# Kernel optimization log

Hardware: AMD Instinct MI355X
Metric: run time of the kernel (lower is better)

The kernel has to match this reference:

```python
import jax, jax.numpy as jnp
import numpy as np

DIM = 768
HEADS = 12
B, N = 1, 4096


def setup_inputs() -> dict:
    key = jax.random.key(0)
    k1, k2, k3 = jax.random.split(key, 3)
    x = jax.random.normal(k1, (B, N, DIM), dtype=jnp.float32)
    W_qkv = jax.random.normal(k2, (DIM, 3 * DIM), dtype=jnp.float32) * (DIM ** -0.5)
    W_out = jax.random.normal(k3, (DIM, DIM), dtype=jnp.float32) * (DIM ** -0.5)
    b_out = jnp.zeros((DIM,), dtype=jnp.float32)
    return {"x": x, "W_qkv": W_qkv, "W_out": W_out, "b_out": b_out}


def reference(x, W_qkv, W_out, b_out):
    b, n, dim = x.shape
    h = HEADS
    d = dim // h
    qkv = x @ W_qkv  # [b, n, 3*dim]
    q, k, v = jnp.split(qkv, 3, axis=-1)
    # 'b n (h d) -> b h n d'
    def to_heads(a):
        return a.reshape(b, n, h, d).transpose(0, 2, 1, 3)
    q, k, v = to_heads(q), to_heads(k), to_heads(v)
    # NOTE: original module computes self.scale but never applies it -> unscaled dots
    dots = jnp.einsum('bhid,bhjd->bhij', q, k)
    attn = jax.nn.softmax(dots, axis=-1)
    out = jnp.einsum('bhij,bhjd->bhid', attn, v)
    out = out.transpose(0, 2, 1, 3).reshape(b, n, dim)  # 'b h n d -> b n (h d)'
    return out @ W_out + b_out
```

## Files before the change

kernel.cpp:

```cpp
#include <hip/hip_runtime.h>

typedef unsigned short ushort_t;
typedef unsigned int uint_t;
typedef __bf16 bf16x8 __attribute__((ext_vector_type(8)));
typedef __bf16 bf16x4 __attribute__((ext_vector_type(4)));
typedef float f32x4 __attribute__((ext_vector_type(4)));
typedef ushort_t u16x4 __attribute__((ext_vector_type(4)));

#define NSEQ 4096
#define DIMM 768
#define NQKV 2304
#define HEADS 12
#define LOG2E 1.4426950408889634f

#if __has_builtin(__builtin_amdgcn_exp2f)
#define EXP2(x) __builtin_amdgcn_exp2f(x)
#else
#define EXP2(x) exp2f(x)
#endif


__device__ __forceinline__ ushort_t f2bf(float f) {
    uint_t u = __float_as_uint(f);
    u = u + 0x7fffu + ((u >> 16) & 1u);
    return (ushort_t)(u >> 16);
}
__device__ __forceinline__ f32x4 zero4() {
    f32x4 v = {0.f, 0.f, 0.f, 0.f};
    return v;
}

__device__ __forceinline__ void gload_lds16(const ushort_t* g, ushort_t* l) {
    __builtin_amdgcn_global_load_lds(
        (const __attribute__((address_space(1))) void*)g,
        (__attribute__((address_space(3))) void*)l, 16, 0, 0);
}

__device__ __forceinline__ void pack_w_tile(const float* __restrict__ src,
                                            ushort_t* __restrict__ dst,
                                            int K, int N, int bk, int bn, int t,
                                            ushort_t* Ls) {
    const int tr = t >> 4, tc = t & 15;
#pragma unroll
    for (int i = 0; i < 4; ++i) {
        int r = tr + 16 * i;
        float4 v = *(const float4*)(&src[(size_t)(bk + r) * N + bn + tc * 4]);
        const float* vv = (const float*)&v;
#pragma unroll
        for (int j = 0; j < 4; ++j) Ls[(tc * 4 + j) * 72 + r] = f2bf(vv[j]);
    }
    __syncthreads();
    const int KB = K >> 3;
    const int n = t >> 2;
    const int ks = t & 3;
    const int gn = bn + n;
    size_t base = ((size_t)(gn >> 4) * KB + ((bk + ks * 16) >> 3)) * 128 + (gn & 15) * 8;
    *(uint4*)(&dst[base])       = *(const uint4*)(&Ls[n * 72 + ks * 16]);
    *(uint4*)(&dst[base + 128]) = *(const uint4*)(&Ls[n * 72 + ks * 16 + 8]);
}

#define CVT_BLOCKS   3072
#define PW1_BLOCKS   (12 * 36)
#define PW2_BLOCKS   (12 * 12)

__global__ __launch_bounds__(256) void prep_kernel(
    const float* __restrict__ X, const float* __restrict__ Wqkv, const float* __restrict__ Wout,
    ushort_t* __restrict__ Ap, ushort_t* __restrict__ Wqp, ushort_t* __restrict__ Wop)
{
    __shared__ ushort_t Ls[64 * 72];
    const int b = blockIdx.x;
    const int t = threadIdx.x;
    if (b < CVT_BLOCKS) {
        int i = b * 256 + t;
        int row = i / (DIMM / 4);
        int k0 = (i - row * (DIMM / 4)) * 4;
        float4 v = *(const float4*)(&X[(size_t)row * DIMM + k0]);
        u16x4 p = { f2bf(v.x), f2bf(v.y), f2bf(v.z), f2bf(v.w) };
        size_t idx = ((size_t)(row >> 4) * (DIMM / 8) + (k0 >> 3)) * 128 + (row & 15) * 8 + (k0 & 7);
        *(u16x4*)(&Ap[idx]) = p;
    } else if (b < CVT_BLOCKS + PW1_BLOCKS) {
        int j = b - CVT_BLOCKS;
        pack_w_tile(Wqkv, Wqp, DIMM, NQKV, (j % 12) * 64, (j / 12) * 64, t, Ls);
    } else {
        int j = b - CVT_BLOCKS - PW1_BLOCKS;
        pack_w_tile(Wout, Wop, DIMM, DIMM, (j % 12) * 64, (j / 12) * 64, t, Ls);
    }
}

#define QKV_STAGE(buf, kt) do {                                          \
    gload_lds16(asrc0 + (kt) * 512, &As[buf][(w * 2)     * 512]);        \
    gload_lds16(asrc1 + (kt) * 512, &As[buf][(w * 2 + 1) * 512]);        \
    gload_lds16(bsrc0 + (kt) * 512, &Bs[buf][(w * 2)     * 512]);        \
    gload_lds16(bsrc1 + (kt) * 512, &Bs[buf][(w * 2 + 1) * 512]);        \
} while (0)

#define QKV_FRAGS(cur) \
    bf16x8 af[4], bfv[4];                                                \
    _Pragma("unroll")                                                    \
    for (int mi = 0; mi < 4; ++mi)                                       \
        af[mi] = *(const bf16x8*)(&As[cur][aoff + mi * 512 + lfr]);      \
    _Pragma("unroll")                                                    \
    for (int nj = 0; nj < 4; ++nj)                                       \
        bfv[nj] = *(const bf16x8*)(&Bs[cur][boff + nj * 512 + lfr]);

__global__ __launch_bounds__(256) void qkv_gemm_kernel(
    const ushort_t* __restrict__ Ap, const ushort_t* __restrict__ Bp,
    ushort_t* __restrict__ Qp, ushort_t* __restrict__ Kp, ushort_t* __restrict__ Vp)
{
    __shared__ ushort_t As[2][4096], Bs[2][4096];
    const int t = threadIdx.x;
    const int lane = t & 63;
    const int w = t >> 6;
    const int m16 = lane & 15;
    const int g = lane >> 4;
    const int wrow = (w >> 1) * 64;
    const int wcol = (w & 1) * 64;
    const int bm = blockIdx.y * 128;
    const int bn = blockIdx.x * 128;
    const int amb = (bm + wrow) >> 4;
    const int bnb = (bn + wcol) >> 4;
    const int bm16 = bm >> 4;
    const int bn16 = bn >> 4;
    const int KB = DIMM / 8;
    const int which = bn / DIMM;

    const ushort_t* asrc0 = Ap + ((size_t)(bm16 + w * 2)     * KB) * 128 + lane * 8;
    const ushort_t* asrc1 = Ap + ((size_t)(bm16 + w * 2 + 1) * KB) * 128 + lane * 8;
    const ushort_t* bsrc0 = Bp + ((size_t)(bn16 + w * 2)     * KB) * 128 + lane * 8;
    const ushort_t* bsrc1 = Bp + ((size_t)(bn16 + w * 2 + 1) * KB) * 128 + lane * 8;
    const int aoff = (w >> 1) * 2048;
    const int boff = (w & 1) * 2048;
    const int lfr = g * 128 + m16 * 8;

    f32x4 acc[4][4];
#pragma unroll
    for (int i = 0; i < 4; ++i)
#pragma unroll
        for (int j = 0; j < 4; ++j) acc[i][j] = zero4();

    QKV_STAGE(0, 0);
    __syncthreads();

    if (which < 2) {
        for (int kt = 0; kt < 24; ++kt) {
            const int cur = kt & 1;
            if (kt + 1 < 24) QKV_STAGE(cur ^ 1, kt + 1);
            QKV_FRAGS(cur);
#pragma unroll
            for (int mi = 0; mi < 4; ++mi)
#pragma unroll
                for (int nj = 0; nj < 4; ++nj)
                    acc[mi][nj] = __builtin_amdgcn_mfma_f32_16x16x32_bf16(bfv[nj], af[mi], acc[mi][nj], 0, 0, 0);
            __syncthreads();
        }
        ushort_t* dst = (which == 0) ? Qp : Kp;
        const float scale = (which == 0) ? LOG2E : 1.0f;
        const int cb = bn - which * DIMM + wcol;
        const int h = cb >> 6;
        const int ghi = g >> 1, glo = g & 1;
#pragma unroll
        for (int mi = 0; mi < 4; ++mi) {
            int sblk = amb + mi;
#pragma unroll
            for (int nj = 0; nj < 4; ++nj) {
                size_t idx = (((size_t)h * 256 + sblk) * 8 + nj * 2 + ghi) * 128 + m16 * 8 + glo * 4;
                u16x4 pk = { f2bf(acc[mi][nj][0] * scale), f2bf(acc[mi][nj][1] * scale),
                             f2bf(acc[mi][nj][2] * scale), f2bf(acc[mi][nj][3] * scale) };
                *(u16x4*)(&dst[idx]) = pk;
            }
        }
    } else {
        for (int kt = 0; kt < 24; ++kt) {
            const int cur = kt & 1;
            if (kt + 1 < 24) QKV_STAGE(cur ^ 1, kt + 1);
            QKV_FRAGS(cur);
#pragma unroll
            for (int mi = 0; mi < 4; ++mi)
#pragma unroll
                for (int nj = 0; nj < 4; ++nj)
                    acc[mi][nj] = __builtin_amdgcn_mfma_f32_16x16x32_bf16(af[mi], bfv[nj], acc[mi][nj], 0, 0, 0);
            __syncthreads();
        }
        const int cb = bn - 2 * DIMM + wcol;
        const int h = cb >> 6;
        const int ghi = g >> 1, glo = g & 1;
        const int kb8 = (bm + wrow) >> 3;
#pragma unroll
        for (int mi = 0; mi < 4; ++mi) {
#pragma unroll
            for (int nj = 0; nj < 4; ++nj) {
                size_t idx = (((size_t)h * 512 + kb8 + mi * 2 + ghi) * 4 + nj) * 128 + m16 * 8 + glo * 4;
                u16x4 pk = { f2bf(acc[mi][nj][0]), f2bf(acc[mi][nj][1]),
                             f2bf(acc[mi][nj][2]), f2bf(acc[mi][nj][3]) };
                *(u16x4*)(&Vp[idx]) = pk;
            }
        }
    }
}

#define ATTN_LOADK(dst, ptr) do {                          \
    dst[0][0] = *(const bf16x8*)(ptr);                     \
    dst[0][1] = *(const bf16x8*)((ptr) + 512);             \
    dst[1][0] = *(const bf16x8*)((ptr) + 1024);            \
    dst[1][1] = *(const bf16x8*)((ptr) + 1536);            \
} while (0)

#define ATTN_LOADV(dst, ptr) do {                          \
    dst[0] = *(const bf16x8*)(ptr);                        \
    dst[1] = *(const bf16x8*)((ptr) + 128);                \
    dst[2] = *(const bf16x8*)((ptr) + 256);                \
    dst[3] = *(const bf16x8*)((ptr) + 384);                \
} while (0)

__global__ __launch_bounds__(128, 3) void attn_kernel(
    const ushort_t* __restrict__ Qp, const ushort_t* __restrict__ Kp,
    const ushort_t* __restrict__ Vp, float* __restrict__ Opart, float* __restrict__ Lpart,
    int niter)
{
    __shared__ ushort_t Ps[2][64 * 40];
    const int t = threadIdx.x;
    const int lane = t & 63;
    const int w = t >> 6;
    const int m16 = lane & 15;
    const int g = lane >> 4;
    const int h = blockIdx.y;
    const int half = blockIdx.z;
    const int qb = blockIdx.x * 128 + w * 64;
    const int qblk0 = qb >> 4;
    const int kblk0 = half * niter * 4;
    const int vblk0 = half * niter * 8;

    bf16x8 qf[4][2];
#pragma unroll
    for (int mi = 0; mi < 4; ++mi)
#pragma unroll
        for (int kd = 0; kd < 2; ++kd)
            qf[mi][kd] = *(const bf16x8*)(&Qp[(((size_t)h * 256 + qblk0 + mi) * 8 + kd * 4 + g) * 128 + m16 * 8]);

    const ushort_t* kp = Kp + ((size_t)h * 256 + kblk0) * 1024 + g * 128 + m16 * 8;
    const ushort_t* vp = Vp + ((size_t)h * 512 + vblk0) * 512 + g * 512 + m16 * 8;

    f32x4 oacc[4][4];
#pragma unroll
    for (int mi = 0; mi < 4; ++mi)
#pragma unroll
        for (int dj = 0; dj < 4; ++dj) oacc[mi][dj] = zero4();
    f32x4 lacc[4] = {zero4(), zero4(), zero4(), zero4()};

    const int nsteps = niter * 2;
    for (int s = 0; s < nsteps; ++s) {
        bf16x8 kf[2][2], vf[4];
        ATTN_LOADK(kf, kp); kp += 2048;
        ATTN_LOADV(vf, vp); vp += 2048;
        asm volatile("" ::: "memory");
#pragma unroll
        for (int mi = 0; mi < 4; ++mi) {
#pragma unroll
            for (int nj = 0; nj < 2; ++nj) {
                f32x4 st = zero4();
                st = __builtin_amdgcn_mfma_f32_16x16x32_bf16(kf[nj][0], qf[mi][0], st, 0, 0, 0);
                st = __builtin_amdgcn_mfma_f32_16x16x32_bf16(kf[nj][1], qf[mi][1], st, 0, 0, 0);
                f32x4 p;
#pragma unroll
                for (int r = 0; r < 4; ++r) p[r] = EXP2(st[r]);
                lacc[mi] += p;
                bf16x4 pk = { (__bf16)p[0], (__bf16)p[1], (__bf16)p[2], (__bf16)p[3] };
                *(bf16x4*)(&Ps[w][(mi * 16 + m16) * 40 + nj * 16 + g * 4]) = pk;
            }
            bf16x8 pf = *(const bf16x8*)(&Ps[w][(mi * 16 + m16) * 40 + g * 8]);
#pragma unroll
            for (int dj = 0; dj < 4; ++dj)
                oacc[mi][dj] = __builtin_amdgcn_mfma_f32_16x16x32_bf16(pf, vf[dj], oacc[mi][dj], 0, 0, 0);
        }
    }

    float* Oph = Opart + (size_t)half * NSEQ * DIMM;
    float* Lph = Lpart + (size_t)half * HEADS * NSEQ + (size_t)h * NSEQ;
#pragma unroll
    for (int mi = 0; mi < 4; ++mi) {
        float l = (lacc[mi][0] + lacc[mi][1]) + (lacc[mi][2] + lacc[mi][3]);
        l += __shfl_xor(l, 16);
        l += __shfl_xor(l, 32);
        if (g == 0) Lph[qb + mi * 16 + m16] = l;
    }
#pragma unroll
    for (int mi = 0; mi < 4; ++mi) {
#pragma unroll
        for (int r = 0; r < 4; ++r) {
            int row = qb + mi * 16 + g * 4 + r;
#pragma unroll
            for (int dj = 0; dj < 4; ++dj)
                Oph[(size_t)row * DIMM + h * 64 + dj * 16 + m16] = oacc[mi][dj][r];
        }
    }
}

__global__ __launch_bounds__(256) void merge_kernel(
    const float* __restrict__ Opart, const float* __restrict__ Lpart,
    ushort_t* __restrict__ Xap, int nsplit)
{
    int i = blockIdx.x * 256 + threadIdx.x;
    int row = i / (DIMM / 4);
    int col0 = (i - row * (DIMM / 4)) * 4;
    int h = col0 >> 6;
    float l = 0.f;
    f32x4 o = zero4();
    for (int s = 0; s < nsplit; ++s) {
        l += Lpart[(size_t)s * HEADS * NSEQ + (size_t)h * NSEQ + row];
        f32x4 ov = *(const f32x4*)(&Opart[(size_t)s * NSEQ * DIMM + (size_t)row * DIMM + col0]);
        o += ov;
    }
    float inv = 1.0f / l;
    u16x4 p = { f2bf(o[0] * inv), f2bf(o[1] * inv), f2bf(o[2] * inv), f2bf(o[3] * inv) };
    size_t idx = ((size_t)(row >> 4) * (DIMM / 8) + (col0 >> 3)) * 128 + (row & 15) * 8 + (col0 & 7);
    *(u16x4*)(&Xap[idx]) = p;
}

__global__ __launch_bounds__(64, 4) void out_gemm_kernel(
    const ushort_t* __restrict__ Ap, const ushort_t* __restrict__ Bp,
    const float* __restrict__ bias, float* __restrict__ out)
{
    const int lane = threadIdx.x & 63;
    const int m16 = lane & 15;
    const int g = lane >> 4;
    const int bm = blockIdx.y * 32;
    const int bn = blockIdx.x * 64;
    const int amb = bm >> 4;
    const int bnb = bn >> 4;
    const int KB = DIMM / 8;

    f32x4 acc[2][4];
#pragma unroll
    for (int i = 0; i < 2; ++i)
#pragma unroll
        for (int j = 0; j < 4; ++j) acc[i][j] = zero4();

#pragma unroll 2
    for (int kt = 0; kt < 24; ++kt) {
        bf16x8 af[2], bfv[4];
#pragma unroll
        for (int mi = 0; mi < 2; ++mi)
            af[mi] = *(const bf16x8*)(&Ap[((size_t)(amb + mi) * KB + kt * 4 + g) * 128 + m16 * 8]);
#pragma unroll
        for (int nj = 0; nj < 4; ++nj)
            bfv[nj] = *(const bf16x8*)(&Bp[((size_t)(bnb + nj) * KB + kt * 4 + g) * 128 + m16 * 8]);
#pragma unroll
        for (int mi = 0; mi < 2; ++mi)
#pragma unroll
            for (int nj = 0; nj < 4; ++nj)
                acc[mi][nj] = __builtin_amdgcn_mfma_f32_16x16x32_bf16(af[mi], bfv[nj], acc[mi][nj], 0, 0, 0);
    }
#pragma unroll
    for (int mi = 0; mi < 2; ++mi) {
#pragma unroll
        for (int nj = 0; nj < 4; ++nj) {
            int col = bn + nj * 16 + m16;
            float bv = bias[col];
#pragma unroll
            for (int r = 0; r < 4; ++r) {
                int row = bm + mi * 16 + g * 4 + r;
                out[(size_t)row * DIMM + col] = acc[mi][nj][r] + bv;
            }
        }
    }
}

extern "C" void kernel_launch(void* const* d_in, const int* in_sizes, int n_in,
                              void* d_out, int out_size, void* d_ws, size_t ws_size,
                              hipStream_t stream) {
    (void)in_sizes; (void)n_in; (void)out_size;
    const float* X    = (const float*)d_in[0];
    const float* Wqkv = (const float*)d_in[1];
    const float* Wout = (const float*)d_in[2];
    const float* bout = (const float*)d_in[3];
    float* out = (float*)d_out;

    const size_t TSZ = (size_t)NSEQ * DIMM;
    const size_t fixed = TSZ * 2 * 5 + (size_t)NQKV * DIMM * 2 + (size_t)DIMM * DIMM * 2;
    const size_t per_split = TSZ * 4 + (size_t)HEADS * NSEQ * 4;
    const int nsplit = (ws_size >= fixed + 4 * per_split) ? 4 : 2;

    unsigned char* p = (unsigned char*)d_ws;
    ushort_t* Ap  = (ushort_t*)p; p += TSZ * 2;
    ushort_t* Wqp = (ushort_t*)p; p += (size_t)NQKV * DIMM * 2;
    ushort_t* Wop = (ushort_t*)p; p += (size_t)DIMM * DIMM * 2;
    ushort_t* Qp  = (ushort_t*)p; p += TSZ * 2;
    ushort_t* Kp  = (ushort_t*)p; p += TSZ * 2;
    ushort_t* Vp  = (ushort_t*)p; p += TSZ * 2;
    ushort_t* Xap = (ushort_t*)p; p += TSZ * 2;
    float* Opart  = (float*)p;    p += (size_t)nsplit * TSZ * 4;
    float* Lpart  = (float*)p;

    const int niter = (NSEQ / 64) / nsplit;

    prep_kernel<<<CVT_BLOCKS + PW1_BLOCKS + PW2_BLOCKS, 256, 0, stream>>>(X, Wqkv, Wout, Ap, Wqp, Wop);
    qkv_gemm_kernel<<<dim3(NQKV / 128, NSEQ / 128), 256, 0, stream>>>(Ap, Wqp, Qp, Kp, Vp);
    attn_kernel<<<dim3(NSEQ / 128, HEADS, nsplit), 128, 0, stream>>>(Qp, Kp, Vp, Opart, Lpart, niter);
    merge_kernel<<<TSZ / 4 / 256, 256, 0, stream>>>(Opart, Lpart, Xap, nsplit);
    out_gemm_kernel<<<dim3(DIMM / 64, NSEQ / 32), 64, 0, stream>>>(Xap, Wop, bout, out);
}
```

Measured before the change: 190.3 us.

## Double-buffer K tiles in LDS via async global-to-LDS loads

K fragments are now prefetched one step ahead into a per-wave double-buffered LDS region using direct global-to-LDS loads. Explicit vmcnt waits split the K wait from the V wait, so K latency overlaps the previous step's work. The QK/softmax pass over all row blocks is now separated from the PV MFMA pass, giving V loads more time to arrive. The cost is extra LDS use, which may reduce occupancy, and a final prefetch that reads one tile past the end of the range.

New measurement: 191.3 us. About the same (+0.5%).

```diff
diff --git a/kernel.cpp b/kernel.cpp
--- a/kernel.cpp
+++ b/kernel.cpp
@@ -198,25 +198,12 @@
     }
 }
 
-#define ATTN_LOADK(dst, ptr) do {                          \
-    dst[0][0] = *(const bf16x8*)(ptr);                     \
-    dst[0][1] = *(const bf16x8*)((ptr) + 512);             \
-    dst[1][0] = *(const bf16x8*)((ptr) + 1024);            \
-    dst[1][1] = *(const bf16x8*)((ptr) + 1536);            \
-} while (0)
-
-#define ATTN_LOADV(dst, ptr) do {                          \
-    dst[0] = *(const bf16x8*)(ptr);                        \
-    dst[1] = *(const bf16x8*)((ptr) + 128);                \
-    dst[2] = *(const bf16x8*)((ptr) + 256);                \
-    dst[3] = *(const bf16x8*)((ptr) + 384);                \
-} while (0)
-
 __global__ __launch_bounds__(128, 3) void attn_kernel(
     const ushort_t* __restrict__ Qp, const ushort_t* __restrict__ Kp,
     const ushort_t* __restrict__ Vp, float* __restrict__ Opart, float* __restrict__ Lpart,
     int niter)
 {
+    __shared__ ushort_t Kst[2][2][2048];
     __shared__ ushort_t Ps[2][64 * 40];
     const int t = threadIdx.x;
     const int lane = t & 63;
@@ -237,7 +224,7 @@
         for (int kd = 0; kd < 2; ++kd)
             qf[mi][kd] = *(const bf16x8*)(&Qp[(((size_t)h * 256 + qblk0 + mi) * 8 + kd * 4 + g) * 128 + m16 * 8]);
 
-    const ushort_t* kp = Kp + ((size_t)h * 256 + kblk0) * 1024 + g * 128 + m16 * 8;
+    const ushort_t* ksrc = Kp + ((size_t)h * 256 + kblk0) * 1024 + lane * 8;
     const ushort_t* vp = Vp + ((size_t)h * 512 + vblk0) * 512 + g * 512 + m16 * 8;
 
     f32x4 oacc[4][4];
@@ -248,11 +235,29 @@
     f32x4 lacc[4] = {zero4(), zero4(), zero4(), zero4()};
 
     const int nsteps = niter * 2;
+#pragma unroll
+    for (int j = 0; j < 4; ++j) gload_lds16(ksrc + j * 512, &Kst[w][0][j * 512]);
+    ksrc += 2048;
+
     for (int s = 0; s < nsteps; ++s) {
-        bf16x8 kf[2][2], vf[4];
-        ATTN_LOADK(kf, kp); kp += 2048;
-        ATTN_LOADV(vf, vp); vp += 2048;
-        asm volatile("" ::: "memory");
+        bf16x8 vf[4];
+        vf[0] = *(const bf16x8*)(vp);
+        vf[1] = *(const bf16x8*)(vp + 128);
+        vf[2] = *(const bf16x8*)(vp + 256);
+        vf[3] = *(const bf16x8*)(vp + 384);
+        vp += 2048;
+#pragma unroll
+        for (int j = 0; j < 4; ++j) gload_lds16(ksrc + j * 512, &Kst[w][(s + 1) & 1][j * 512]);
+        ksrc += 2048;
+        asm volatile("s_waitcnt vmcnt(8)" ::: "memory");
+
+        const ushort_t* kb = &Kst[w][s & 1][lane * 8];
+        bf16x8 kf[2][2];
+        kf[0][0] = *(const bf16x8*)(kb);
+        kf[0][1] = *(const bf16x8*)(kb + 512);
+        kf[1][0] = *(const bf16x8*)(kb + 1024);
+        kf[1][1] = *(const bf16x8*)(kb + 1536);
+
 #pragma unroll
         for (int mi = 0; mi < 4; ++mi) {
 #pragma unroll
@@ -267,12 +272,18 @@
                 bf16x4 pk = { (__bf16)p[0], (__bf16)p[1], (__bf16)p[2], (__bf16)p[3] };
                 *(bf16x4*)(&Ps[w][(mi * 16 + m16) * 40 + nj * 16 + g * 4]) = pk;
             }
+        }
+        asm volatile("s_waitcnt vmcnt(4)" ::: "memory");
+
+#pragma unroll
+        for (int mi = 0; mi < 4; ++mi) {
             bf16x8 pf = *(const bf16x8*)(&Ps[w][(mi * 16 + m16) * 40 + g * 8]);
 #pragma unroll
             for (int dj = 0; dj < 4; ++dj)
                 oacc[mi][dj] = __builtin_amdgcn_mfma_f32_16x16x32_bf16(pf, vf[dj], oacc[mi][dj], 0, 0, 0);
         }
     }
+    asm volatile("s_waitcnt vmcnt(0)" ::: "memory");
 
     float* Oph = Opart + (size_t)half * NSEQ * DIMM;
     float* Lph = Lpart + (size_t)half * HEADS * NSEQ + (size_t)h * NSEQ;
```

## Double-buffer K tiles in LDS via async global-to-LDS loads and prefetch V

Applied to the files above, without the earlier changes.

Restructures the attention inner loop into a two-stage software pipeline. K tiles are copied directly from global memory into a per-wave double-buffered LDS region and V fragments are prefetched into alternating register sets, with manual vmcnt waits so the loads for the next step overlap the MFMA and exp work of the current one. This targets exposed global-load latency in the loop. It adds LDS usage and register pressure, which may lower occupancy. The final prefetch reads past the last tile, and the correctness of the hand-written waitcnt counts depends on how many loads the compiler emits.

Result: slower. 286.6 us (+50.6%).

```diff
diff --git a/kernel.cpp b/kernel.cpp
--- a/kernel.cpp
+++ b/kernel.cpp
@@ -198,18 +198,44 @@
     }
 }
 
-#define ATTN_LOADK(dst, ptr) do {                          \
-    dst[0][0] = *(const bf16x8*)(ptr);                     \
-    dst[0][1] = *(const bf16x8*)((ptr) + 512);             \
-    dst[1][0] = *(const bf16x8*)((ptr) + 1024);            \
-    dst[1][1] = *(const bf16x8*)((ptr) + 1536);            \
+#define ATTN_PREFETCH(VF, KBUF) do {                                     \
+    VF[0] = *(const bf16x8*)(vp);                                        \
+    VF[1] = *(const bf16x8*)(vp + 128);                                  \
+    VF[2] = *(const bf16x8*)(vp + 256);                                  \
+    VF[3] = *(const bf16x8*)(vp + 384);                                  \
+    vp += 2048;                                                          \
+    _Pragma("unroll")                                                    \
+    for (int j = 0; j < 4; ++j)                                          \
+        gload_lds16(ksrc + j * 512, &Kst[w][KBUF][j * 512]);             \
+    ksrc += 2048;                                                        \
 } while (0)
 
-#define ATTN_LOADV(dst, ptr) do {                          \
-    dst[0] = *(const bf16x8*)(ptr);                        \
-    dst[1] = *(const bf16x8*)((ptr) + 128);                \
-    dst[2] = *(const bf16x8*)((ptr) + 256);                \
-    dst[3] = *(const bf16x8*)((ptr) + 384);                \
+#define ATTN_COMPUTE(KBUF, VF) do {                                                           \
+    const ushort_t* kb_ = &Kst[w][KBUF][lane * 8];                                            \
+    bf16x8 kf_[2][2];                                                                         \
+    kf_[0][0] = *(const bf16x8*)(kb_);                                                        \
+    kf_[0][1] = *(const bf16x8*)(kb_ + 512);                                                  \
+    kf_[1][0] = *(const bf16x8*)(kb_ + 1024);                                                 \
+    kf_[1][1] = *(const bf16x8*)(kb_ + 1536);                                                 \
+    _Pragma("unroll")                                                                         \
+    for (int mi = 0; mi < 4; ++mi) {                                                          \
+        _Pragma("unroll")                                                                     \
+        for (int nj = 0; nj < 2; ++nj) {                                                      \
+            f32x4 st = zero4();                                                               \
+            st = __builtin_amdgcn_mfma_f32_16x16x32_bf16(kf_[nj][0], qf[mi][0], st, 0, 0, 0); \
+            st = __builtin_amdgcn_mfma_f32_16x16x32_bf16(kf_[nj][1], qf[mi][1], st, 0, 0, 0); \
+            f32x4 p;                                                                          \
+            _Pragma("unroll")                                                                 \
+            for (int r = 0; r < 4; ++r) p[r] = EXP2(st[r]);                                   \
+            lacc[mi] += p;                                                                    \
+            bf16x4 pk = { (__bf16)p[0], (__bf16)p[1], (__bf16)p[2], (__bf16)p[3] };           \
+            *(bf16x4*)(&Ps[w][(mi * 16 + m16) * 40 + nj * 16 + g * 4]) = pk;                  \
+        }                                                                                     \
+        bf16x8 pf = *(const bf16x8*)(&Ps[w][(mi * 16 + m16) * 40 + g * 8]);                   \
+        _Pragma("unroll")                                                                     \
+        for (int dj = 0; dj < 4; ++dj)                                                        \
+            oacc[mi][dj] = __builtin_amdgcn_mfma_f32_16x16x32_bf16(pf, VF[dj], oacc[mi][dj], 0, 0, 0); \
+    }                                                                                         \
 } while (0)
 
 __global__ __launch_bounds__(128, 3) void attn_kernel(
@@ -217,6 +243,7 @@
     const ushort_t* __restrict__ Vp, float* __restrict__ Opart, float* __restrict__ Lpart,
     int niter)
 {
+    __shared__ ushort_t Kst[2][2][2048];
     __shared__ ushort_t Ps[2][64 * 40];
     const int t = threadIdx.x;
     const int lane = t & 63;
@@ -237,7 +264,7 @@
         for (int kd = 0; kd < 2; ++kd)
             qf[mi][kd] = *(const bf16x8*)(&Qp[(((size_t)h * 256 + qblk0 + mi) * 8 + kd * 4 + g) * 128 + m16 * 8]);
 
-    const ushort_t* kp = Kp + ((size_t)h * 256 + kblk0) * 1024 + g * 128 + m16 * 8;
+    const ushort_t* ksrc = Kp + ((size_t)h * 256 + kblk0) * 1024 + lane * 8;
     const ushort_t* vp = Vp + ((size_t)h * 512 + vblk0) * 512 + g * 512 + m16 * 8;
 
     f32x4 oacc[4][4];
@@ -248,31 +275,18 @@
     f32x4 lacc[4] = {zero4(), zero4(), zero4(), zero4()};
 
     const int nsteps = niter * 2;
-    for (int s = 0; s < nsteps; ++s) {
-        bf16x8 kf[2][2], vf[4];
-        ATTN_LOADK(kf, kp); kp += 2048;
-        ATTN_LOADV(vf, vp); vp += 2048;
-        asm volatile("" ::: "memory");
-#pragma unroll
-        for (int mi = 0; mi < 4; ++mi) {
-#pragma unroll
-            for (int nj = 0; nj < 2; ++nj) {
-                f32x4 st = zero4();
-                st = __builtin_amdgcn_mfma_f32_16x16x32_bf16(kf[nj][0], qf[mi][0], st, 0, 0, 0);
-                st = __builtin_amdgcn_mfma_f32_16x16x32_bf16(kf[nj][1], qf[mi][1], st, 0, 0, 0);
-                f32x4 p;
-#pragma unroll
-                for (int r = 0; r < 4; ++r) p[r] = EXP2(st[r]);
-                lacc[mi] += p;
-                bf16x4 pk = { (__bf16)p[0], (__bf16)p[1], (__bf16)p[2], (__bf16)p[3] };
-                *(bf16x4*)(&Ps[w][(mi * 16 + m16) * 40 + nj * 16 + g * 4]) = pk;
-            }
-            bf16x8 pf = *(const bf16x8*)(&Ps[w][(mi * 16 + m16) * 40 + g * 8]);
-#pragma unroll
-            for (int dj = 0; dj < 4; ++dj)
-                oacc[mi][dj] = __builtin_amdgcn_mfma_f32_16x16x32_bf16(pf, vf[dj], oacc[mi][dj], 0, 0, 0);
-        }
-    }
+    bf16x8 vA[4], vB[4];
+    ATTN_PREFETCH(vA, 0);
+
+    for (int s = 0; s < nsteps; s += 2) {
+        ATTN_PREFETCH(vB, 1);
+        asm volatile("s_waitcnt vmcnt(8)" ::: "memory");
+        ATTN_COMPUTE(0, vA);
+        ATTN_PREFETCH(vA, 0);
+        asm volatile("s_waitcnt vmcnt(8)" ::: "memory");
+        ATTN_COMPUTE(1, vB);
+    }
+    asm volatile("s_waitcnt vmcnt(0)" ::: "memory");
 
     float* Oph = Opart + (size_t)half * NSEQ * DIMM;
     float* Lph = Lpart + (size_t)half * HEADS * NSEQ + (size_t)h * NSEQ;
```
